# Kernel tuning notes

Hardware: AMD Instinct MI355X
Metric: run time of the kernel (lower is better)

## Reference

```python
import jax, jax.numpy as jnp
import numpy as np

B, T = 256, 2048
U = Y = 32
H = 128
Z = 64
L = 2  # GRU layers


def _mlp2(x, w1, b1, w2, b2):
    # Linear -> ReLU -> Linear (PyTorch Linear: y = x @ W.T + b)
    return jax.nn.relu(x @ w1.T + b1) @ w2.T + b2


def _gru_cell(x, h, wih, whh):
    # PyTorch GRUCell (bias=False), gate order [r, z, n]
    gi = x @ wih.T  # [B, 3H]
    gh = h @ whh.T
    i_r, i_z, i_n = jnp.split(gi, 3, axis=-1)
    h_r, h_z, h_n = jnp.split(gh, 3, axis=-1)
    r = jax.nn.sigmoid(i_r + h_r)
    z = jax.nn.sigmoid(i_z + h_z)
    n = jnp.tanh(i_n + r * h_n)
    return (1.0 - z) * n + z * h


def setup_inputs() -> dict:
    key = jax.random.key(0)
    ks = jax.random.split(key, 32)
    f32 = jnp.float32
    w = lambda k, shape: jax.random.normal(k, shape, f32) * 0.05
    inp = {
        'u': jax.random.normal(ks[0], (B, U, T), f32),
        'y': jax.random.normal(ks[1], (B, Y, T), f32),
        'h0': jax.random.uniform(ks[2], (L, B, H), f32),
        # phi_u: Linear(U,H) ReLU Linear(H,H)
        'pu_w1': w(ks[3], (H, U)), 'pu_b1': w(ks[4], (H,)),
        'pu_w2': w(ks[5], (H, H)), 'pu_b2': w(ks[6], (H,)),
        # dynn: Linear(2H,H) ReLU Linear(H,H)
        'dy_w1': w(ks[7], (H, 2 * H)), 'dy_b1': w(ks[8], (H,)),
        'dy_w2': w(ks[9], (H, H)), 'dy_b2': w(ks[10], (H,)),
        # x_mean / x_logvar heads: Linear(H,Z)
        'xm_w': w(ks[11], (Z, H)), 'xm_b': w(ks[12], (Z,)),
        'xlv_w': w(ks[13], (Z, H)), 'xlv_b': w(ks[14], (Z,)),
        # phi_x: Linear(2Z,H) ReLU Linear(H,H)
        'px_w1': w(ks[15], (H, 2 * Z)), 'px_b1': w(ks[16], (H,)),
        'px_w2': w(ks[17], (H, H)), 'px_b2': w(ks[18], (H,)),
        # menn: Linear(H,H) ReLU Linear(H,Y)
        'me_w1': w(ks[19], (H, H)), 'me_b1': w(ks[20], (H,)),
        'me_w2': w(ks[21], (Y, H)), 'me_b2': w(ks[22], (Y,)),
        # GRU (bias=False), stacked per layer: [L, 3H, H]
        'gru_wih': w(ks[23], (L, 3 * H, H)),
        'gru_whh': w(ks[24], (L, 3 * H, H)),
    }
    return inp


def reference(u, y, h0, pu_w1, pu_b1, pu_w2, pu_b2, dy_w1, dy_b1, dy_w2, dy_b2,
              xm_w, xm_b, xlv_w, xlv_b, px_w1, px_b1, px_w2, px_b2,
              me_w1, me_b1, me_w2, me_b2, gru_wih, gru_whh):
    u_seq = jnp.moveaxis(u, 2, 0)  # [T, B, U]
    y_seq = jnp.moveaxis(y, 2, 0)  # [T, B, Y]

    def step(carry, ty):
        h, loss = carry  # h: [L, B, H]
        ut, yt = ty
        phi_u = _mlp2(ut, pu_w1, pu_b1, pu_w2, pu_b2)                     # [B, H]
        dphi = _mlp2(jnp.concatenate([phi_u, h[-1]], axis=1),
                     dy_w1, dy_b1, dy_w2, dy_b2)                          # [B, H]
        x_mean = dphi @ xm_w.T + xm_b                                     # [B, Z]
        x_logvar = dphi @ xlv_w.T + xlv_b                                 # [B, Z]
        # GRU step (uses pre-update h; dynn already consumed old h[-1])
        inp = phi_u
        new_h = []
        for l in range(L):
            hl = _gru_cell(inp, h[l], gru_wih[l], gru_whh[l])
            new_h.append(hl)
            inp = hl
        h = jnp.stack(new_h)
        # mpnt_wt <= 0 branch: pure NN measurement
        phi_x = _mlp2(jnp.concatenate([x_mean, x_logvar], axis=1),
                      px_w1, px_b1, px_w2, px_b2)                         # [B, H]
        y_hat = _mlp2(phi_x, me_w1, me_b1, me_w2, me_b2)                  # [B, Y]
        loss = loss + jnp.sum((y_hat - yt) ** 2)
        return (h, loss), None

    (h, loss), _ = jax.lax.scan(step, (h0, jnp.float32(0.0)), (u_seq, y_seq))
    return loss
```

## Files before the change

kernel.cpp:

```cpp
#include <hip/hip_runtime.h>

#define DI __device__ __forceinline__

typedef unsigned short u16;
typedef unsigned int u32;
typedef unsigned long long u64;
typedef __bf16 bf16v __attribute__((ext_vector_type(8)));
typedef float f32x4 __attribute__((ext_vector_type(4)));

constexpr int B_ = 256, T_ = 2048, H_ = 128;
constexpr int BU = B_ * 32;

constexpr size_t O_PU_W1 = 0;
constexpr size_t O_PU_W2 = 4096;
constexpr size_t O_DY_W1 = 20480;
constexpr size_t O_DY_W2 = 53248;
constexpr size_t O_XM_W  = 69632;
constexpr size_t O_XLV_W = 77824;
constexpr size_t O_PX_W1 = 86016;
constexpr size_t O_PX_W2 = 102400;
constexpr size_t O_ME_W1 = 118784;
constexpr size_t O_ME_W2 = 135168;
constexpr size_t O_WIH   = 139264;
constexpr size_t O_WHH   = 237568;

constexpr size_t WS_WB   = 0;
constexpr size_t WS_HST  = 0x100000;
constexpr size_t WS_PART = 0x140000;
constexpr size_t WS_DATA = 0x180000;

DI u16 f2b(float x) {
  union { float f; unsigned u; } v; v.f = x;
  unsigned r = v.u + 0x7fffu + ((v.u >> 16) & 1u);
  return (u16)(r >> 16);
}
DI float b2f(u16 h) { union { unsigned u; float f; } v; v.u = ((unsigned)h) << 16; return v.f; }
DI float asf(u32 u) { union { unsigned u; float f; } v; v.u = u; return v.f; }
DI float sigm(float x) {
  return __builtin_amdgcn_rcpf(1.f + __builtin_amdgcn_exp2f(-1.44269504f * x));
}
DI float tanhg(float x) {
  return fmaf(2.f, __builtin_amdgcn_rcpf(1.f + __builtin_amdgcn_exp2f(-2.88539008f * x)), -1.f);
}
DI f32x4 MFMA(bf16v a, bf16v b, f32x4 c) {
  return __builtin_amdgcn_mfma_f32_16x16x32_bf16(a, b, c, 0, 0, 0);
}
DI void MFA(f32x4& c, const bf16v& a_agpr, const bf16v& b) {
  asm("v_mfma_f32_16x16x32_bf16 %0, %1, %2, %0"
      : "+v"(c) : "a"(a_agpr), "v"(b));
}
DI bf16v ldb(const u16* p) { return *reinterpret_cast<const bf16v*>(p); }
DI u32 cvtpk(float a, float b) {
  u32 d;
  asm("v_cvt_pk_bf16_f32 %0, %1, %2" : "=v"(d) : "v"(a), "v"(b));
  return d;
}
DI u64 pk4(float a, float b, float c, float d) {
  return (u64)cvtpk(a, b) | ((u64)cvtpk(c, d) << 32);
}
DI void bar_lds() {
  asm volatile("s_waitcnt lgkmcnt(0)\n\ts_barrier" ::: "memory");
}

__global__ void k_convert_weights(
    const float* pu_w1, const float* pu_w2, const float* dy_w1, const float* dy_w2,
    const float* xm_w, const float* xlv_w, const float* px_w1, const float* px_w2,
    const float* me_w1, const float* me_w2, const float* gih, const float* ghh,
    const float* h0, u16* wb, float* hst) {
  int i0 = blockIdx.x * blockDim.x + threadIdx.x;
  int st = gridDim.x * blockDim.x;
#define CVT(src, off, n) for (int i = i0; i < (n); i += st) wb[(off) + i] = f2b(src[i]);
  CVT(pu_w1, O_PU_W1, 4096)  CVT(pu_w2, O_PU_W2, 16384)
  CVT(dy_w1, O_DY_W1, 32768) CVT(dy_w2, O_DY_W2, 16384)
  CVT(xm_w,  O_XM_W,  8192)  CVT(xlv_w, O_XLV_W, 8192)
  CVT(px_w1, O_PX_W1, 16384) CVT(px_w2, O_PX_W2, 16384)
  CVT(me_w1, O_ME_W1, 16384) CVT(me_w2, O_ME_W2, 4096)
  CVT(gih,   O_WIH,   98304) CVT(ghh,   O_WHH,   98304)
#undef CVT
  for (int i = i0; i < 2 * B_ * H_; i += st) hst[i] = h0[i];
}

__global__ void k_transpose(const float* __restrict__ u, const float* __restrict__ y,
                            u16* __restrict__ uT, u16* __restrict__ yT, int t0) {
  const float* src = blockIdx.z ? y : u;
  u16* dst = blockIdx.z ? yT : uT;
  __shared__ float tile[32][33];
  const int tx = threadIdx.x, ty = threadIdx.y;
  const int c0 = blockIdx.x * 32;
  const int r0 = blockIdx.y * 32;
#pragma unroll
  for (int i = 0; i < 4; ++i)
    tile[ty + i * 8][tx] = src[(size_t)(r0 + ty + i * 8) * T_ + t0 + c0 + tx];
  __syncthreads();
#pragma unroll
  for (int i = 0; i < 4; ++i)
    dst[(size_t)(c0 + ty + i * 8) * BU + r0 + tx] = f2b(tile[tx][ty + i * 8]);
}

DI void role_gru(u16* smem, const u16* __restrict__ gi0, const u16* __restrict__ wb,
                 float* __restrict__ hst, u16* __restrict__ h1old, int TCr, int blk) {
  u16* SH0 = smem;
  u16* SH1 = smem + 4352;
  const int lane = threadIdx.x & 63, w = threadIdx.x >> 6;
  const int ln = lane & 15, lq = lane >> 4;
  const int f0 = w * 16;
  const int fme = f0 + lq * 4;
  const int b0 = blk * 16;
  const u16* wh0 = wb + O_WHH;
  const u16* wi1 = wb + O_WIH + 49152;
  const u16* wh1 = wb + O_WHH + 49152;

  bf16v wH0[3][4], wI1[3][4], wH1[3][4];
#pragma unroll
  for (int g = 0; g < 3; ++g)
#pragma unroll
    for (int kt = 0; kt < 4; ++kt) {
      size_t row = (size_t)(g * 128 + f0 + ln);
      size_t col = (size_t)kt * 32 + lq * 8;
      wH0[g][kt] = ldb(wh0 + row * H_ + col);
      wI1[g][kt] = ldb(wi1 + row * H_ + col);
      wH1[g][kt] = ldb(wh1 + row * H_ + col);
    }
#pragma unroll
  for (int g = 0; g < 3; ++g)
#pragma unroll
    for (int kt = 0; kt < 4; ++kt)
      asm volatile("" : "+a"(wH0[g][kt]), "+a"(wI1[g][kt]), "+a"(wH1[g][kt]));

  float h0s[4], h1s[4];
#pragma unroll
  for (int j = 0; j < 4; ++j) {
    h0s[j] = hst[(size_t)(0 * B_ + b0 + ln) * H_ + fme + j];
    h1s[j] = hst[(size_t)(1 * B_ + b0 + ln) * H_ + fme + j];
  }
  *reinterpret_cast<u64*>(&SH0[2176 + ln * 136 + fme]) = pk4(h0s[0], h0s[1], h0s[2], h0s[3]);
  *reinterpret_cast<u64*>(&SH1[2176 + ln * 136 + fme]) = pk4(h1s[0], h1s[1], h1s[2], h1s[3]);
  u16* hp = h1old + (size_t)(b0 + ln) * H_ + fme;
  *reinterpret_cast<u64*>(hp) = pk4(h1s[0], h1s[1], h1s[2], h1s[3]);

  const u16* gp = gi0 + (size_t)(b0 + ln) * 384 + fme;
  u64 gq0 = *reinterpret_cast<const u64*>(gp);
  u64 gq1 = *reinterpret_cast<const u64*>(gp + 128);
  u64 gq2 = *reinterpret_cast<const u64*>(gp + 256);
  gp += (size_t)B_ * 384;

  __syncthreads();

  {
    f32x4 cR = {0,0,0,0}, cZ = {0,0,0,0}, cHN = {0,0,0,0};
#pragma unroll
    for (int kt = 0; kt < 4; ++kt) {
      bf16v aH = ldb(&SH0[2176 + ln * 136 + kt * 32 + lq * 8]);
      MFA(cR,  wH0[0][kt], aH);
      MFA(cZ,  wH0[1][kt], aH);
      MFA(cHN, wH0[2][kt], aH);
    }
    u32 l0 = (u32)gq0, h0w = (u32)(gq0 >> 32);
    u32 l1 = (u32)gq1, h1w = (u32)(gq1 >> 32);
    u32 l2 = (u32)gq2, h2w = (u32)(gq2 >> 32);
    float gr[4] = {asf(l0 << 16), asf(l0 & 0xffff0000u), asf(h0w << 16), asf(h0w & 0xffff0000u)};
    float gz[4] = {asf(l1 << 16), asf(l1 & 0xffff0000u), asf(h1w << 16), asf(h1w & 0xffff0000u)};
    float gn[4] = {asf(l2 << 16), asf(l2 & 0xffff0000u), asf(h2w << 16), asf(h2w & 0xffff0000u)};
#pragma unroll
    for (int j = 0; j < 4; ++j) {
      float r = sigm(cR[j] + gr[j]);
      float z = sigm(cZ[j] + gz[j]);
      float n = tanhg(fmaf(r, cHN[j], gn[j]));
      h0s[j] = fmaf(z, h0s[j] - n, n);
    }
    *reinterpret_cast<u64*>(&SH0[0 * 2176 + ln * 136 + fme]) =
        pk4(h0s[0], h0s[1], h0s[2], h0s[3]);
    gq0 = *reinterpret_cast<const u64*>(gp);
    gq1 = *reinterpret_cast<const u64*>(gp + 128);
    gq2 = *reinterpret_cast<const u64*>(gp + 256);
    gp += (size_t)B_ * 384;
    bar_lds();
  }

#define GRU_PERIOD(H0R, H0W, DOL0, SLOT_OK, PF)                                 \
  {                                                                             \
    bf16v aH[4], aG[4];                                                         \
    _Pragma("unroll")                                                           \
    for (int kt = 0; kt < 4; ++kt) {                                            \
      aH[kt] = ldb(&SH0[(H0R) * 2176 + ln * 136 + kt * 32 + lq * 8]);           \
      aG[kt] = ldb(&SH1[(H0W) * 2176 + ln * 136 + kt * 32 + lq * 8]);           \
    }                                                                           \
    f32x4 dR = {0,0,0,0}, dZ = {0,0,0,0}, dIN = {0,0,0,0}, dHN = {0,0,0,0};     \
    _Pragma("unroll")                                                           \
    for (int kt = 0; kt < 4; ++kt) {                                            \
      MFA(dR,  wI1[0][kt], aH[kt]);  MFA(dR,  wH1[0][kt], aG[kt]);              \
      MFA(dZ,  wI1[1][kt], aH[kt]);  MFA(dZ,  wH1[1][kt], aG[kt]);              \
      MFA(dIN, wI1[2][kt], aH[kt]);  MFA(dHN, wH1[2][kt], aG[kt]);              \
    }                                                                           \
    if (DOL0) {                                                                 \
      f32x4 cR = {0,0,0,0}, cZ = {0,0,0,0}, cHN = {0,0,0,0};                    \
      _Pragma("unroll")                                                         \
      for (int kt = 0; kt < 4; ++kt) {                                          \
        MFA(cR,  wH0[0][kt], aH[kt]);                                           \
        MFA(cZ,  wH0[1][kt], aH[kt]);                                           \
        MFA(cHN, wH0[2][kt], aH[kt]);                                           \
      }                                                                         \
      u32 l0 = (u32)gq0, h0w = (u32)(gq0 >> 32);                                \
      u32 l1 = (u32)gq1, h1w = (u32)(gq1 >> 32);                                \
      u32 l2 = (u32)gq2, h2w = (u32)(gq2 >> 32);                                \
      float gr[4] = {asf(l0 << 16), asf(l0 & 0xffff0000u),                      \
                     asf(h0w << 16), asf(h0w & 0xffff0000u)};                   \
      float gz[4] = {asf(l1 << 16), asf(l1 & 0xffff0000u),                      \
                     asf(h1w << 16), asf(h1w & 0xffff0000u)};                   \
      float gn[4] = {asf(l2 << 16), asf(l2 & 0xffff0000u),                      \
                     asf(h2w << 16), asf(h2w & 0xffff0000u)};                   \
      _Pragma("unroll")                                                         \
      for (int j = 0; j < 4; ++j) {                                             \
        float r = sigm(cR[j] + gr[j]);                                          \
        float z = sigm(cZ[j] + gz[j]);                                          \
        float n = tanhg(fmaf(r, cHN[j], gn[j]));                                \
        h0s[j] = fmaf(z, h0s[j] - n, n);                                        \
      }                                                                         \
      *reinterpret_cast<u64*>(&SH0[(H0W) * 2176 + ln * 136 + fme]) =            \
          pk4(h0s[0], h0s[1], h0s[2], h0s[3]);                                  \
    }                                                                           \
    {                                                                           \
      _Pragma("unroll")                                                         \
      for (int j = 0; j < 4; ++j) {                                             \
        float r = sigm(dR[j]);                                                  \
        float z = sigm(dZ[j]);                                                  \
        float n = tanhg(fmaf(r, dHN[j], dIN[j]));                               \
        h1s[j] = fmaf(z, h1s[j] - n, n);                                        \
      }                                                                         \
      u64 q = pk4(h1s[0], h1s[1], h1s[2], h1s[3]);                              \
      *reinterpret_cast<u64*>(&SH1[(H0R) * 2176 + ln * 136 + fme]) = q;         \
      if (SLOT_OK) {                                                            \
        hp += (size_t)B_ * H_;                                                  \
        *reinterpret_cast<u64*>(hp) = q;                                        \
      }                                                                         \
    }                                                                           \
    if (PF) {                                                                   \
      gq0 = *reinterpret_cast<const u64*>(gp);                                  \
      gq1 = *reinterpret_cast<const u64*>(gp + 128);                            \
      gq2 = *reinterpret_cast<const u64*>(gp + 256);                            \
      gp += (size_t)B_ * 384;                                                   \
    }                                                                           \
    bar_lds();                                                                  \
  }

  for (int s = 1; s <= TCr; s += 2) {
    GRU_PERIOD(0, 1, true, true, (s + 1 < TCr))
    GRU_PERIOD(1, 0, (s + 1 < TCr), (s + 1 < TCr), (s + 2 < TCr))
  }
#undef GRU_PERIOD

#pragma unroll
  for (int j = 0; j < 4; ++j) {
    hst[(size_t)(0 * B_ + b0 + ln) * H_ + fme + j] = h0s[j];
    hst[(size_t)(1 * B_ + b0 + ln) * H_ + fme + j] = h1s[j];
  }
}

DI void layer128(const u16* __restrict__ W, const float* __restrict__ bias,
                 const u16* A, u16* Dst, int dstOff, int nTiles, bool relu,
                 int ln, int lq) {
  bf16v a[2][4];
#pragma unroll
  for (int mt = 0; mt < 2; ++mt)
#pragma unroll
    for (int kt = 0; kt < 4; ++kt)
      a[mt][kt] = ldb(A + (mt * 16 + ln) * 136 + kt * 32 + lq * 8);
  for (int nt = 0; nt < nTiles; ++nt) {
    f32x4 c0 = {0,0,0,0}, c1 = {0,0,0,0};
#pragma unroll
    for (int kt = 0; kt < 4; ++kt) {
      bf16v b = ldb(W + (nt * 16 + ln) * 128 + kt * 32 + lq * 8);
      c0 = MFMA(a[0][kt], b, c0); c1 = MFMA(a[1][kt], b, c1);
    }
    float bv = bias[nt * 16 + ln];
#pragma unroll
    for (int mt = 0; mt < 2; ++mt)
#pragma unroll
      for (int j = 0; j < 4; ++j) {
        float v = (mt ? c1[j] : c0[j]) + bv;
        if (relu) v = fmaxf(v, 0.f);
        Dst[(mt * 16 + lq * 4 + j) * 136 + dstOff + nt * 16 + ln] = f2b(v);
      }
  }
}

DI void role_post(u16* smem, const u16* __restrict__ phiu, const u16* __restrict__ h1old,
                  const u16* __restrict__ yT, const u16* __restrict__ wb,
                  const float* dy_b1, const float* dy_b2, const float* xm_b,
                  const float* xlv_b, const float* px_b1, const float* px_b2,
                  const float* me_b1, const float* me_b2,
                  float* __restrict__ partials, int first, int blk) {
  const int lane = threadIdx.x & 63, w = threadIdx.x >> 6;
  const int ln = lane & 15, lq = lane >> 4;
  const int r0 = (blk * 8 + w) * 32;
  u16* X = smem + w * 8704;
  u16* Yb = X + 4352;
  float* wsum = (float*)(smem + 69632);

  {
    bf16v a[2][8];
#pragma unroll
    for (int mt = 0; mt < 2; ++mt)
#pragma unroll
      for (int kt = 0; kt < 8; ++kt) {
        size_t row = (size_t)(r0 + mt * 16 + ln);
        a[mt][kt] = (kt < 4) ? ldb(phiu + row * H_ + kt * 32 + lq * 8)
                             : ldb(h1old + row * H_ + (kt - 4) * 32 + lq * 8);
      }
    const u16* W = wb + O_DY_W1;
    for (int nt = 0; nt < 8; ++nt) {
      f32x4 c0 = {0,0,0,0}, c1 = {0,0,0,0};
#pragma unroll
      for (int kt = 0; kt < 8; ++kt) {
        bf16v b = ldb(W + (nt * 16 + ln) * 256 + kt * 32 + lq * 8);
        c0 = MFMA(a[0][kt], b, c0); c1 = MFMA(a[1][kt], b, c1);
      }
      float bv = dy_b1[nt * 16 + ln];
#pragma unroll
      for (int mt = 0; mt < 2; ++mt)
#pragma unroll
        for (int j = 0; j < 4; ++j) {
          float v = (mt ? c1[j] : c0[j]) + bv;
          X[(mt * 16 + lq * 4 + j) * 136 + nt * 16 + ln] = f2b(fmaxf(v, 0.f));
        }
    }
  }
  layer128(wb + O_DY_W2, dy_b2, X, Yb, 0, 8, false, ln, lq);
  layer128(wb + O_XM_W,  xm_b,  Yb, X, 0, 4, false, ln, lq);
  layer128(wb + O_XLV_W, xlv_b, Yb, X, 64, 4, false, ln, lq);
  layer128(wb + O_PX_W1, px_b1, X, Yb, 0, 8, true,  ln, lq);
  layer128(wb + O_PX_W2, px_b2, Yb, X, 0, 8, false, ln, lq);
  layer128(wb + O_ME_W1, me_b1, X, Yb, 0, 8, true,  ln, lq);

  float lsum = 0.f;
  {
    bf16v a[2][4];
#pragma unroll
    for (int mt = 0; mt < 2; ++mt)
#pragma unroll
      for (int kt = 0; kt < 4; ++kt)
        a[mt][kt] = ldb(Yb + (mt * 16 + ln) * 136 + kt * 32 + lq * 8);
    const u16* W = wb + O_ME_W2;
#pragma unroll
    for (int nt = 0; nt < 2; ++nt) {
      f32x4 c0 = {0,0,0,0}, c1 = {0,0,0,0};
#pragma unroll
      for (int kt = 0; kt < 4; ++kt) {
        bf16v b = ldb(W + (nt * 16 + ln) * 128 + kt * 32 + lq * 8);
        c0 = MFMA(a[0][kt], b, c0); c1 = MFMA(a[1][kt], b, c1);
      }
      float bv = me_b2[nt * 16 + ln];
#pragma unroll
      for (int mt = 0; mt < 2; ++mt)
#pragma unroll
        for (int j = 0; j < 4; ++j) {
          int m = mt * 16 + lq * 4 + j;
          float v = (mt ? c1[j] : c0[j]) + bv;
          float yv = b2f(yT[(size_t)(r0 + m) * 32 + nt * 16 + ln]);
          float d = v - yv;
          lsum += d * d;
        }
    }
  }
#pragma unroll
  for (int o = 32; o; o >>= 1) lsum += __shfl_down(lsum, o);
  if (lane == 0) wsum[w] = lsum;
  __syncthreads();
  if (threadIdx.x == 0) {
    float v = 0.f;
#pragma unroll
    for (int i = 0; i < 8; ++i) v += wsum[i];
    if (first) partials[blk] = v;
    else       partials[blk] += v;
  }
}

DI void role_phiu(u16* smem, const u16* __restrict__ uT, const u16* __restrict__ wb,
                  const float* __restrict__ pu_b1, const float* __restrict__ pu_b2,
                  u16* __restrict__ phiu, u16* __restrict__ gi0, int blk) {
  const int lane = threadIdx.x & 63, w = threadIdx.x >> 6;
  const int ln = lane & 15, lq = lane >> 4;
  const int r0 = (blk * 8 + w) * 32;
  u16* hb  = smem + w * 4352;
  u16* hb2 = smem + 34816 + w * 4352;

  bf16v a0 = ldb(uT + (size_t)(r0 + ln) * 32 + lq * 8);
  bf16v a1 = ldb(uT + (size_t)(r0 + 16 + ln) * 32 + lq * 8);
  const u16* w1 = wb + O_PU_W1;
#pragma unroll
  for (int nt = 0; nt < 8; ++nt) {
    f32x4 c0 = {0.f, 0.f, 0.f, 0.f}, c1 = {0.f, 0.f, 0.f, 0.f};
    bf16v b = ldb(w1 + (nt * 16 + ln) * 32 + lq * 8);
    c0 = MFMA(a0, b, c0); c1 = MFMA(a1, b, c1);
    float bv = pu_b1[nt * 16 + ln];
#pragma unroll
    for (int j = 0; j < 4; ++j) {
      hb[(lq * 4 + j) * 136 + nt * 16 + ln]      = f2b(fmaxf(c0[j] + bv, 0.f));
      hb[(16 + lq * 4 + j) * 136 + nt * 16 + ln] = f2b(fmaxf(c1[j] + bv, 0.f));
    }
  }
  bf16v a[2][4];
#pragma unroll
  for (int mt = 0; mt < 2; ++mt)
#pragma unroll
    for (int kt = 0; kt < 4; ++kt)
      a[mt][kt] = ldb(hb + (mt * 16 + ln) * 136 + kt * 32 + lq * 8);
  const u16* w2 = wb + O_PU_W2;
#pragma unroll
  for (int nt = 0; nt < 8; ++nt) {
    f32x4 c0 = {0.f, 0.f, 0.f, 0.f}, c1 = {0.f, 0.f, 0.f, 0.f};
#pragma unroll
    for (int kt = 0; kt < 4; ++kt) {
      bf16v b = ldb(w2 + (nt * 16 + ln) * 128 + kt * 32 + lq * 8);
      c0 = MFMA(a[0][kt], b, c0); c1 = MFMA(a[1][kt], b, c1);
    }
    float bv = pu_b2[nt * 16 + ln];
#pragma unroll
    for (int mt = 0; mt < 2; ++mt)
#pragma unroll
      for (int j = 0; j < 4; ++j) {
        float v = (mt ? c1[j] : c0[j]) + bv;
        hb2[(mt * 16 + lq * 4 + j) * 136 + nt * 16 + ln] = f2b(v);
      }
  }
  __syncthreads();

#pragma unroll
  for (int i = 0; i < 16; ++i) {
    int idx = lane + 64 * i;
    int row = idx >> 5, c4 = idx & 31;
    u64 v = *reinterpret_cast<const u64*>(&hb2[row * 136 + c4 * 4]);
    *reinterpret_cast<u64*>(&phiu[(size_t)(r0 + row) * 128 + c4 * 4]) = v;
  }

  bf16v bP[2][4];
#pragma unroll
  for (int bh = 0; bh < 2; ++bh)
#pragma unroll
    for (int kt = 0; kt < 4; ++kt)
      bP[bh][kt] = ldb(&hb2[(bh * 16 + ln) * 136 + kt * 32 + lq * 8]);
  const u16* wih0 = wb + O_WIH;
  for (int nt = 0; nt < 24; ++nt) {
    bf16v aW[4];
#pragma unroll
    for (int kt = 0; kt < 4; ++kt)
      aW[kt] = ldb(wih0 + (size_t)(nt * 16 + ln) * 128 + kt * 32 + lq * 8);
#pragma unroll
    for (int bh = 0; bh < 2; ++bh) {
      f32x4 c = {0.f, 0.f, 0.f, 0.f};
#pragma unroll
      for (int kt = 0; kt < 4; ++kt) c = MFMA(aW[kt], bP[bh][kt], c);
      u64 q = pk4(c[0], c[1], c[2], c[3]);
      *reinterpret_cast<u64*>(
          &gi0[(size_t)(r0 + bh * 16 + ln) * 384 + nt * 16 + lq * 4]) = q;
    }
  }
}

DI void role_transpose(u16* smem, const float* __restrict__ u, const float* __restrict__ y,
                       u16* __restrict__ uT, u16* __restrict__ yT, int t0, int blk, int TCr) {
  float* tile = (float*)smem;
  const int worker = threadIdx.x >> 8;
  const int tid = threadIdx.x & 255;
  const int tx = tid & 31, ty = tid >> 5;
  float* tl = tile + worker * (32 * 33);
  const int ntt = TCr / 32;
  for (int i = 0; i < 4; ++i) {
    int gtile = blk * 8 + worker * 4 + i;
    int tt = gtile % ntt;
    int rest = gtile / ntt;
    int rr = rest & 255, uy = rest >> 8;
    const float* src = uy ? y : u;
    u16* dst = uy ? yT : uT;
    int c0 = tt * 32, r0 = rr * 32;
#pragma unroll
    for (int k = 0; k < 4; ++k)
      tl[(ty + k * 8) * 33 + tx] = src[(size_t)(r0 + ty + k * 8) * T_ + t0 + c0 + tx];
    __syncthreads();
#pragma unroll
    for (int k = 0; k < 4; ++k)
      dst[(size_t)(c0 + ty + k * 8) * BU + r0 + tx] = f2b(tl[tx * 33 + ty + k * 8]);
    __syncthreads();
  }
}

__global__ __launch_bounds__(512, 2) void k_mega(
    const float* u, const float* yy,
    const u16* uT_r, u16* uT_w, u16* yT_w, const u16* yT_r,
    const u16* phiu_r, u16* phiu_w,
    const u16* gi0_r, u16* gi0_w,
    const u16* h1_r, u16* h1_w,
    const u16* wb, float* hst,
    const float* pu_b1, const float* pu_b2,
    const float* dy_b1, const float* dy_b2, const float* xm_b, const float* xlv_b,
    const float* px_b1, const float* px_b2, const float* me_b1, const float* me_b2,
    float* partials, int first,
    int TCr, int nG, int nP, int nU, int t0T) {
  __shared__ __align__(16) u16 smem[69664];
  int b = blockIdx.x;
  if (b < nG) { role_gru(smem, gi0_r, wb, hst, h1_w, TCr, b); return; }
  b -= nG;
  if (b < nP) {
    role_post(smem, phiu_r, h1_r, yT_r, wb, dy_b1, dy_b2, xm_b, xlv_b,
              px_b1, px_b2, me_b1, me_b2, partials, first, b);
    return;
  }
  b -= nP;
  if (b < nU) { role_phiu(smem, uT_r, wb, pu_b1, pu_b2, phiu_w, gi0_w, b); return; }
  b -= nU;
  role_transpose(smem, u, yy, uT_w, yT_w, t0T, b, TCr);
}

__global__ void k_finalize(const float* __restrict__ partials, float* __restrict__ out,
                           int nPart) {
  __shared__ double s[256];
  double acc = 0.0;
  for (int i = threadIdx.x; i < nPart; i += 256) acc += (double)partials[i];
  s[threadIdx.x] = acc;
  __syncthreads();
  for (int o = 128; o; o >>= 1) {
    if (threadIdx.x < o) s[threadIdx.x] += s[threadIdx.x + o];
    __syncthreads();
  }
  if (threadIdx.x == 0) out[0] = (float)s[0];
}

extern "C" void kernel_launch(void* const* d_in, const int* in_sizes, int n_in,
                              void* d_out, int out_size, void* d_ws, size_t ws_size,
                              hipStream_t stream) {
  const float* u     = (const float*)d_in[0];
  const float* y     = (const float*)d_in[1];
  const float* h0    = (const float*)d_in[2];
  const float* pu_w1 = (const float*)d_in[3];
  const float* pu_b1 = (const float*)d_in[4];
  const float* pu_w2 = (const float*)d_in[5];
  const float* pu_b2 = (const float*)d_in[6];
  const float* dy_w1 = (const float*)d_in[7];
  const float* dy_b1 = (const float*)d_in[8];
  const float* dy_w2 = (const float*)d_in[9];
  const float* dy_b2 = (const float*)d_in[10];
  const float* xm_w  = (const float*)d_in[11];
  const float* xm_b  = (const float*)d_in[12];
  const float* xlv_w = (const float*)d_in[13];
  const float* xlv_b = (const float*)d_in[14];
  const float* px_w1 = (const float*)d_in[15];
  const float* px_b1 = (const float*)d_in[16];
  const float* px_w2 = (const float*)d_in[17];
  const float* px_b2 = (const float*)d_in[18];
  const float* me_w1 = (const float*)d_in[19];
  const float* me_b1 = (const float*)d_in[20];
  const float* me_w2 = (const float*)d_in[21];
  const float* me_b2 = (const float*)d_in[22];
  const float* gih   = (const float*)d_in[23];
  const float* ghh   = (const float*)d_in[24];

  int TC = 64;
  for (int cand : {256, 128}) {
    size_t ut = (size_t)cand * B_ * 32 * 2;
    size_t ph = (size_t)cand * B_ * 128 * 2;
    size_t gi = (size_t)cand * B_ * 384 * 2;
    if (WS_DATA + 6 * ut + 5 * ph + 2 * gi <= ws_size) { TC = cand; break; }
  }
  const int NCH = T_ / TC;
  const int RC = TC * B_;
  size_t ut_b = (size_t)RC * 32 * 2, ph_b = (size_t)RC * 128 * 2, gi_b = (size_t)RC * 384 * 2;

  char* ws = (char*)d_ws;
  u16* wb    = (u16*)(ws + WS_WB);
  float* hst = (float*)(ws + WS_HST);
  float* prt = (float*)(ws + WS_PART);
  char* p = ws + WS_DATA;
  u16* uTb[2]; u16* yTb[4]; u16* phb[3]; u16* h1b[2]; u16* gib[2];
  for (int i = 0; i < 2; ++i) { uTb[i] = (u16*)p; p += ut_b; }
  for (int i = 0; i < 4; ++i) { yTb[i] = (u16*)p; p += ut_b; }
  for (int i = 0; i < 3; ++i) { phb[i] = (u16*)p; p += ph_b; }
  for (int i = 0; i < 2; ++i) { h1b[i] = (u16*)p; p += ph_b; }
  for (int i = 0; i < 2; ++i) { gib[i] = (u16*)p; p += gi_b; }
  float* out = (float*)d_out;

  const int nPostB = RC / 256;
  const int nPhiB  = RC / 256;
  const int nTrB   = (TC / 32) * 64;

  k_convert_weights<<<256, 256, 0, stream>>>(pu_w1, pu_w2, dy_w1, dy_w2, xm_w, xlv_w,
                                             px_w1, px_w2, me_w1, me_w2, gih, ghh,
                                             h0, wb, hst);
  k_transpose<<<dim3(TC / 32, 256, 2), dim3(32, 8), 0, stream>>>(u, y, uTb[0], yTb[0], 0);
  if (NCH > 1)
    k_transpose<<<dim3(TC / 32, 256, 2), dim3(32, 8), 0, stream>>>(u, y, uTb[1], yTb[1], TC);
  k_mega<<<nPhiB, 512, 0, stream>>>(u, y, uTb[0], uTb[0], yTb[0], yTb[0],
                                    phb[0], phb[0], gib[0], gib[0], h1b[0], h1b[0],
                                    wb, hst, pu_b1, pu_b2, dy_b1, dy_b2, xm_b, xlv_b,
                                    px_b1, px_b2, me_b1, me_b2, prt, 0,
                                    TC, 0, 0, nPhiB, 0);
  for (int c = 0; c <= NCH; ++c) {
    int nG = (c < NCH) ? 16 : 0;
    int nP = (c >= 1) ? nPostB : 0;
    int nU = (c + 1 < NCH) ? nPhiB : 0;
    int nT = (c + 2 < NCH) ? nTrB : 0;
    int grid = nG + nP + nU + nT;
    if (!grid) continue;
    k_mega<<<grid, 512, 0, stream>>>(
        u, y,
        uTb[(c + 1) & 1], uTb[(c + 2) & 1], yTb[(c + 2) & 3],
        yTb[c >= 1 ? (c - 1) & 3 : 0],
        phb[c >= 1 ? (c - 1) % 3 : 0], phb[(c + 1) % 3],
        gib[c & 1], gib[(c + 1) & 1],
        h1b[c >= 1 ? (c - 1) & 1 : 0], h1b[c & 1],
        wb, hst, pu_b1, pu_b2, dy_b1, dy_b2, xm_b, xlv_b,
        px_b1, px_b2, me_b1, me_b2,
        prt, (c == 1) ? 1 : 0,
        TC, nG, nP, nU, (c + 2) * TC);
  }
  k_finalize<<<1, 256, 0, stream>>>(prt, out, nPostB);
}
```

Before: 2.752 ms.

## Split GRU layers into separate producer/consumer blocks synchronized via global flags

The two GRU layers, previously computed together in each recurrence block, now run in separate workgroups. Sixteen layer-0 blocks compute h0 and publish it to a global buffer with a release flag per step. Sixteen layer-1 blocks spin on that flag and consume h0 from global memory. This shortens the serial per-step critical path and spreads register and MFMA load across twice as many CUs. In exchange it adds global-memory round trips and spin-wait latency per step, plus a deadlock risk if the producer blocks are not co-resident with the consumers.

```diff
diff --git a/kernel.cpp b/kernel.cpp
--- a/kernel.cpp
+++ b/kernel.cpp
@@ -27,6 +27,7 @@
 constexpr size_t WS_WB   = 0;
 constexpr size_t WS_HST  = 0x100000;
 constexpr size_t WS_PART = 0x140000;
+constexpr size_t WS_FLAG = 0x150000;
 constexpr size_t WS_DATA = 0x180000;
 
 DI u16 f2b(float x) {
@@ -66,7 +67,7 @@
     const float* pu_w1, const float* pu_w2, const float* dy_w1, const float* dy_w2,
     const float* xm_w, const float* xlv_w, const float* px_w1, const float* px_w2,
     const float* me_w1, const float* me_w2, const float* gih, const float* ghh,
-    const float* h0, u16* wb, float* hst) {
+    const float* h0, u16* wb, float* hst, u32* flags) {
   int i0 = blockIdx.x * blockDim.x + threadIdx.x;
   int st = gridDim.x * blockDim.x;
 #define CVT(src, off, n) for (int i = i0; i < (n); i += st) wb[(off) + i] = f2b(src[i]);
@@ -78,6 +79,7 @@
   CVT(gih,   O_WIH,   98304) CVT(ghh,   O_WHH,   98304)
 #undef CVT
   for (int i = i0; i < 2 * B_ * H_; i += st) hst[i] = h0[i];
+  for (int i = i0; i < 16; i += st) flags[i] = 0;
 }
 
 __global__ void k_transpose(const float* __restrict__ u, const float* __restrict__ y,
@@ -97,46 +99,34 @@
     dst[(size_t)(c0 + ty + i * 8) * BU + r0 + tx] = f2b(tile[tx][ty + i * 8]);
 }
 
-DI void role_gru(u16* smem, const u16* __restrict__ gi0, const u16* __restrict__ wb,
-                 float* __restrict__ hst, u16* __restrict__ h1old, int TCr, int blk) {
+DI void role_gru0(u16* smem, const u16* __restrict__ gi0, const u16* __restrict__ wb,
+                  float* __restrict__ hst, u16* __restrict__ h0x, u32* flags,
+                  int pbase, int TCr, int blk) {
   u16* SH0 = smem;
-  u16* SH1 = smem + 4352;
   const int lane = threadIdx.x & 63, w = threadIdx.x >> 6;
   const int ln = lane & 15, lq = lane >> 4;
   const int f0 = w * 16;
   const int fme = f0 + lq * 4;
   const int b0 = blk * 16;
   const u16* wh0 = wb + O_WHH;
-  const u16* wi1 = wb + O_WIH + 49152;
-  const u16* wh1 = wb + O_WHH + 49152;
-
-  bf16v wH0[3][4], wI1[3][4], wH1[3][4];
+
+  bf16v wH0[3][4];
 #pragma unroll
   for (int g = 0; g < 3; ++g)
 #pragma unroll
-    for (int kt = 0; kt < 4; ++kt) {
-      size_t row = (size_t)(g * 128 + f0 + ln);
-      size_t col = (size_t)kt * 32 + lq * 8;
-      wH0[g][kt] = ldb(wh0 + row * H_ + col);
-      wI1[g][kt] = ldb(wi1 + row * H_ + col);
-      wH1[g][kt] = ldb(wh1 + row * H_ + col);
-    }
+    for (int kt = 0; kt < 4; ++kt)
+      wH0[g][kt] = ldb(wh0 + (size_t)(g * 128 + f0 + ln) * H_ + kt * 32 + lq * 8);
 #pragma unroll
   for (int g = 0; g < 3; ++g)
 #pragma unroll
     for (int kt = 0; kt < 4; ++kt)
-      asm volatile("" : "+a"(wH0[g][kt]), "+a"(wI1[g][kt]), "+a"(wH1[g][kt]));
-
-  float h0s[4], h1s[4];
-#pragma unroll
-  for (int j = 0; j < 4; ++j) {
+      asm volatile("" : "+a"(wH0[g][kt]));
+
+  float h0s[4];
+#pragma unroll
+  for (int j = 0; j < 4; ++j)
     h0s[j] = hst[(size_t)(0 * B_ + b0 + ln) * H_ + fme + j];
-    h1s[j] = hst[(size_t)(1 * B_ + b0 + ln) * H_ + fme + j];
-  }
   *reinterpret_cast<u64*>(&SH0[2176 + ln * 136 + fme]) = pk4(h0s[0], h0s[1], h0s[2], h0s[3]);
-  *reinterpret_cast<u64*>(&SH1[2176 + ln * 136 + fme]) = pk4(h1s[0], h1s[1], h1s[2], h1s[3]);
-  u16* hp = h1old + (size_t)(b0 + ln) * H_ + fme;
-  *reinterpret_cast<u64*>(hp) = pk4(h1s[0], h1s[1], h1s[2], h1s[3]);
 
   const u16* gp = gi0 + (size_t)(b0 + ln) * 384 + fme;
   u64 gq0 = *reinterpret_cast<const u64*>(gp);
@@ -146,14 +136,19 @@
 
   __syncthreads();
 
-  {
+  u16* rd = SH0 + 2176;
+  u16* wr = SH0;
+  for (int s = 0; s < TCr; ++s) {
+    bf16v aH[4];
+#pragma unroll
+    for (int kt = 0; kt < 4; ++kt)
+      aH[kt] = ldb(&rd[ln * 136 + kt * 32 + lq * 8]);
     f32x4 cR = {0,0,0,0}, cZ = {0,0,0,0}, cHN = {0,0,0,0};
 #pragma unroll
     for (int kt = 0; kt < 4; ++kt) {
-      bf16v aH = ldb(&SH0[2176 + ln * 136 + kt * 32 + lq * 8]);
-      MFA(cR,  wH0[0][kt], aH);
-      MFA(cZ,  wH0[1][kt], aH);
-      MFA(cHN, wH0[2][kt], aH);
+      MFA(cR,  wH0[0][kt], aH[kt]);
+      MFA(cZ,  wH0[1][kt], aH[kt]);
+      MFA(cHN, wH0[2][kt], aH[kt]);
     }
     u32 l0 = (u32)gq0, h0w = (u32)(gq0 >> 32);
     u32 l1 = (u32)gq1, h1w = (u32)(gq1 >> 32);
@@ -168,92 +163,127 @@
       float n = tanhg(fmaf(r, cHN[j], gn[j]));
       h0s[j] = fmaf(z, h0s[j] - n, n);
     }
-    *reinterpret_cast<u64*>(&SH0[0 * 2176 + ln * 136 + fme]) =
-        pk4(h0s[0], h0s[1], h0s[2], h0s[3]);
-    gq0 = *reinterpret_cast<const u64*>(gp);
-    gq1 = *reinterpret_cast<const u64*>(gp + 128);
-    gq2 = *reinterpret_cast<const u64*>(gp + 256);
-    gp += (size_t)B_ * 384;
+    u64 q = pk4(h0s[0], h0s[1], h0s[2], h0s[3]);
+    __hip_atomic_store(
+        (unsigned long long*)(h0x + (size_t)s * B_ * H_ + (size_t)(b0 + ln) * H_ + fme),
+        q, __ATOMIC_RELAXED, __HIP_MEMORY_SCOPE_AGENT);
+    *reinterpret_cast<u64*>(&wr[ln * 136 + fme]) = q;
+    __syncthreads();
+    if (threadIdx.x == 0)
+      __hip_atomic_store(&flags[blk], (u32)(pbase + s + 1),
+                         __ATOMIC_RELEASE, __HIP_MEMORY_SCOPE_AGENT);
+    if (s + 1 < TCr) {
+      gq0 = *reinterpret_cast<const u64*>(gp);
+      gq1 = *reinterpret_cast<const u64*>(gp + 128);
+      gq2 = *reinterpret_cast<const u64*>(gp + 256);
+      gp += (size_t)B_ * 384;
+    }
+    u16* tmp = rd; rd = wr; wr = tmp;
+  }
+#pragma unroll
+  for (int j = 0; j < 4; ++j)
+    hst[(size_t)(0 * B_ + b0 + ln) * H_ + fme + j] = h0s[j];
+}
+
+DI void role_gru1(u16* smem, const u16* __restrict__ wb,
+                  float* __restrict__ hst, u16* __restrict__ h1old,
+                  const u16* __restrict__ h0x, u32* flags,
+                  int pbase, int TCr, int blk) {
+  u16* SH1 = smem;
+  const int lane = threadIdx.x & 63, w = threadIdx.x >> 6;
+  const int ln = lane & 15, lq = lane >> 4;
+  const int f0 = w * 16;
+  const int fme = f0 + lq * 4;
+  const int b0 = blk * 16;
+  const u16* wi1 = wb + O_WIH + 49152;
+  const u16* wh1 = wb + O_WHH + 49152;
+
+  bf16v wI1[3][4], wH1[3][4];
+#pragma unroll
+  for (int g = 0; g < 3; ++g)
+#pragma unroll
+    for (int kt = 0; kt < 4; ++kt) {
+      size_t row = (size_t)(g * 128 + f0 + ln);
+      size_t col = (size_t)kt * 32 + lq * 8;
+      wI1[g][kt] = ldb(wi1 + row * H_ + col);
+      wH1[g][kt] = ldb(wh1 + row * H_ + col);
+    }
+#pragma unroll
+  for (int g = 0; g < 3; ++g)
+#pragma unroll
+    for (int kt = 0; kt < 4; ++kt)
+      asm volatile("" : "+a"(wI1[g][kt]), "+a"(wH1[g][kt]));
+
+  float h1s[4];
+#pragma unroll
+  for (int j = 0; j < 4; ++j)
+    h1s[j] = hst[(size_t)(1 * B_ + b0 + ln) * H_ + fme + j];
+  u64 qi = pk4(h1s[0], h1s[1], h1s[2], h1s[3]);
+  *reinterpret_cast<u64*>(&SH1[2176 + ln * 136 + fme]) = qi;
+  u16* hp = h1old + (size_t)(b0 + ln) * H_ + fme;
+  *reinterpret_cast<u64*>(hp) = qi;
+
+  __syncthreads();
+
+  u16* rd = SH1 + 2176;
+  u16* wr = SH1;
+  u32 seen = 0;
+  for (int s = 1; s <= TCr; ++s) {
+    u32 want = (u32)(pbase + s);
+    if (seen < want) {
+      do {
+        seen = __hip_atomic_load(&flags[blk], __ATOMIC_RELAXED, __HIP_MEMORY_SCOPE_AGENT);
+      } while (seen < want);
+      __builtin_amdgcn_fence(__ATOMIC_ACQUIRE, "agent");
+    }
+    const unsigned long long* hsrc = (const unsigned long long*)
+        (h0x + (size_t)(s - 1) * B_ * H_ + (size_t)(b0 + ln) * H_);
+    bf16v aH[4];
+#pragma unroll
+    for (int kt = 0; kt < 4; ++kt) {
+      union { u64 q[2]; bf16v v; } t;
+      t.q[0] = __hip_atomic_load((unsigned long long*)(hsrc + kt * 8 + lq * 2),
+                                 __ATOMIC_RELAXED, __HIP_MEMORY_SCOPE_AGENT);
+      t.q[1] = __hip_atomic_load((unsigned long long*)(hsrc + kt * 8 + lq * 2 + 1),
+                                 __ATOMIC_RELAXED, __HIP_MEMORY_SCOPE_AGENT);
+      aH[kt] = t.v;
+    }
+    bf16v aG[4];
+#pragma unroll
+    for (int kt = 0; kt < 4; ++kt)
+      aG[kt] = ldb(&rd[ln * 136 + kt * 32 + lq * 8]);
+    f32x4 dR = {0,0,0,0}, dZ = {0,0,0,0}, dIN = {0,0,0,0}, dHN = {0,0,0,0};
+#pragma unroll
+    for (int kt = 0; kt < 4; ++kt) {
+      MFA(dR,  wH1[0][kt], aG[kt]);
+      MFA(dZ,  wH1[1][kt], aG[kt]);
+      MFA(dHN, wH1[2][kt], aG[kt]);
+    }
+#pragma unroll
+    for (int kt = 0; kt < 4; ++kt) {
+      MFA(dR,  wI1[0][kt], aH[kt]);
+      MFA(dZ,  wI1[1][kt], aH[kt]);
+      MFA(dIN, wI1[2][kt], aH[kt]);
+    }
+#pragma unroll
+    for (int j = 0; j < 4; ++j) {
+      float r = sigm(dR[j]);
+      float z = sigm(dZ[j]);
+      float n = tanhg(fmaf(r, dHN[j], dIN[j]));
+      h1s[j] = fmaf(z, h1s[j] - n, n);
+    }
+    u64 q = pk4(h1s[0], h1s[1], h1s[2], h1s[3]);
+    *reinterpret_cast<u64*>(&wr[ln * 136 + fme]) = q;
+    if (s < TCr) {
+      hp += (size_t)B_ * H_;
+      *reinterpret_cast<u64*>(hp) = q;
+    }
     bar_lds();
-  }
-
-#define GRU_PERIOD(H0R, H0W, DOL0, SLOT_OK, PF)                                 \
-  {                                                                             \
-    bf16v aH[4], aG[4];                                                         \
-    _Pragma("unroll")                                                           \
-    for (int kt = 0; kt < 4; ++kt) {                                            \
-      aH[kt] = ldb(&SH0[(H0R) * 2176 + ln * 136 + kt * 32 + lq * 8]);           \
-      aG[kt] = ldb(&SH1[(H0W) * 2176 + ln * 136 + kt * 32 + lq * 8]);           \
-    }                                                                           \
-    f32x4 dR = {0,0,0,0}, dZ = {0,0,0,0}, dIN = {0,0,0,0}, dHN = {0,0,0,0};     \
-    _Pragma("unroll")                                                           \
-    for (int kt = 0; kt < 4; ++kt) {                                            \
-      MFA(dR,  wI1[0][kt], aH[kt]);  MFA(dR,  wH1[0][kt], aG[kt]);              \
-      MFA(dZ,  wI1[1][kt], aH[kt]);  MFA(dZ,  wH1[1][kt], aG[kt]);              \
-      MFA(dIN, wI1[2][kt], aH[kt]);  MFA(dHN, wH1[2][kt], aG[kt]);              \
-    }                                                                           \
-    if (DOL0) {                                                                 \
-      f32x4 cR = {0,0,0,0}, cZ = {0,0,0,0}, cHN = {0,0,0,0};                    \
-      _Pragma("unroll")                                                         \
-      for (int kt = 0; kt < 4; ++kt) {                                          \
-        MFA(cR,  wH0[0][kt], aH[kt]);                                           \
-        MFA(cZ,  wH0[1][kt], aH[kt]);                                           \
-        MFA(cHN, wH0[2][kt], aH[kt]);                                           \
-      }                                                                         \
-      u32 l0 = (u32)gq0, h0w = (u32)(gq0 >> 32);                                \
-      u32 l1 = (u32)gq1, h1w = (u32)(gq1 >> 32);                                \
-      u32 l2 = (u32)gq2, h2w = (u32)(gq2 >> 32);                                \
-      float gr[4] = {asf(l0 << 16), asf(l0 & 0xffff0000u),                      \
-                     asf(h0w << 16), asf(h0w & 0xffff0000u)};                   \
-      float gz[4] = {asf(l1 << 16), asf(l1 & 0xffff0000u),                      \
-                     asf(h1w << 16), asf(h1w & 0xffff0000u)};                   \
-      float gn[4] = {asf(l2 << 16), asf(l2 & 0xffff0000u),                      \
-                     asf(h2w << 16), asf(h2w & 0xffff0000u)};                   \
-      _Pragma("unroll")                                                         \
-      for (int j = 0; j < 4; ++j) {                                             \
-        float r = sigm(cR[j] + gr[j]);                                          \
-        float z = sigm(cZ[j] + gz[j]);                                          \
-        float n = tanhg(fmaf(r, cHN[j], gn[j]));                                \
-        h0s[j] = fmaf(z, h0s[j] - n, n);                                        \
-      }                                                                         \
-      *reinterpret_cast<u64*>(&SH0[(H0W) * 2176 + ln * 136 + fme]) =            \
-          pk4(h0s[0], h0s[1], h0s[2], h0s[3]);                                  \
-    }                                                                           \
-    {                                                                           \
-      _Pragma("unroll")                                                         \
-      for (int j = 0; j < 4; ++j) {                                             \
-        float r = sigm(dR[j]);                                                  \
-        float z = sigm(dZ[j]);                                                  \
-        float n = tanhg(fmaf(r, dHN[j], dIN[j]));                               \
-        h1s[j] = fmaf(z, h1s[j] - n, n);                                        \
-      }                                                                         \
-      u64 q = pk4(h1s[0], h1s[1], h1s[2], h1s[3]);                              \
-      *reinterpret_cast<u64*>(&SH1[(H0R) * 2176 + ln * 136 + fme]) = q;         \
-      if (SLOT_OK) {                                                            \
-        hp += (size_t)B_ * H_;                                                  \
-        *reinterpret_cast<u64*>(hp) = q;                                        \
-      }                                                                         \
-    }                                                                           \
-    if (PF) {                                                                   \
-      gq0 = *reinterpret_cast<const u64*>(gp);                                  \
-      gq1 = *reinterpret_cast<const u64*>(gp + 128);                            \
-      gq2 = *reinterpret_cast<const u64*>(gp + 256);                            \
-      gp += (size_t)B_ * 384;                                                   \
-    }                                                                           \
-    bar_lds();                                                                  \
-  }
-
-  for (int s = 1; s <= TCr; s += 2) {
-    GRU_PERIOD(0, 1, true, true, (s + 1 < TCr))
-    GRU_PERIOD(1, 0, (s + 1 < TCr), (s + 1 < TCr), (s + 2 < TCr))
-  }
-#undef GRU_PERIOD
-
-#pragma unroll
-  for (int j = 0; j < 4; ++j) {
-    hst[(size_t)(0 * B_ + b0 + ln) * H_ + fme + j] = h0s[j];
+    u16* tmp = rd; rd = wr; wr = tmp;
+  }
+#pragma unroll
+  for (int j = 0; j < 4; ++j)
     hst[(size_t)(1 * B_ + b0 + ln) * H_ + fme + j] = h1s[j];
-  }
 }
 
 DI void layer128(const u16* __restrict__ W, const float* __restrict__ bias,
@@ -490,6 +520,7 @@
     const u16* phiu_r, u16* phiu_w,
     const u16* gi0_r, u16* gi0_w,
     const u16* h1_r, u16* h1_w,
+    u16* h0x, u32* flags, int pbase,
     const u16* wb, float* hst,
     const float* pu_b1, const float* pu_b2,
     const float* dy_b1, const float* dy_b2, const float* xm_b, const float* xlv_b,
@@ -498,7 +529,11 @@
     int TCr, int nG, int nP, int nU, int t0T) {
   __shared__ __align__(16) u16 smem[69664];
   int b = blockIdx.x;
-  if (b < nG) { role_gru(smem, gi0_r, wb, hst, h1_w, TCr, b); return; }
+  if (b < nG) {
+    if (b < 16) role_gru0(smem, gi0_r, wb, hst, h0x, flags, pbase, TCr, b);
+    else        role_gru1(smem, wb, hst, h1_w, h0x, flags, pbase, TCr, b - 16);
+    return;
+  }
   b -= nG;
   if (b < nP) {
     role_post(smem, phiu_r, h1_r, yT_r, wb, dy_b1, dy_b2, xm_b, xlv_b,
@@ -559,7 +594,7 @@
     size_t ut = (size_t)cand * B_ * 32 * 2;
     size_t ph = (size_t)cand * B_ * 128 * 2;
     size_t gi = (size_t)cand * B_ * 384 * 2;
-    if (WS_DATA + 6 * ut + 5 * ph + 2 * gi <= ws_size) { TC = cand; break; }
+    if (WS_DATA + 6 * ut + 6 * ph + 2 * gi <= ws_size) { TC = cand; break; }
   }
   const int NCH = T_ / TC;
   const int RC = TC * B_;
@@ -569,13 +604,15 @@
   u16* wb    = (u16*)(ws + WS_WB);
   float* hst = (float*)(ws + WS_HST);
   float* prt = (float*)(ws + WS_PART);
+  u32* flg   = (u32*)(ws + WS_FLAG);
   char* p = ws + WS_DATA;
-  u16* uTb[2]; u16* yTb[4]; u16* phb[3]; u16* h1b[2]; u16* gib[2];
+  u16* uTb[2]; u16* yTb[4]; u16* phb[3]; u16* h1b[2]; u16* gib[2]; u16* h0x;
   for (int i = 0; i < 2; ++i) { uTb[i] = (u16*)p; p += ut_b; }
   for (int i = 0; i < 4; ++i) { yTb[i] = (u16*)p; p += ut_b; }
   for (int i = 0; i < 3; ++i) { phb[i] = (u16*)p; p += ph_b; }
   for (int i = 0; i < 2; ++i) { h1b[i] = (u16*)p; p += ph_b; }
   for (int i = 0; i < 2; ++i) { gib[i] = (u16*)p; p += gi_b; }
+  h0x = (u16*)p; p += ph_b;
   float* out = (float*)d_out;
 
   const int nPostB = RC / 256;
@@ -584,17 +621,18 @@
 
   k_convert_weights<<<256, 256, 0, stream>>>(pu_w1, pu_w2, dy_w1, dy_w2, xm_w, xlv_w,
                                              px_w1, px_w2, me_w1, me_w2, gih, ghh,
-                                             h0, wb, hst);
+                                             h0, wb, hst, flg);
   k_transpose<<<dim3(TC / 32, 256, 2), dim3(32, 8), 0, stream>>>(u, y, uTb[0], yTb[0], 0);
   if (NCH > 1)
     k_transpose<<<dim3(TC / 32, 256, 2), dim3(32, 8), 0, stream>>>(u, y, uTb[1], yTb[1], TC);
   k_mega<<<nPhiB, 512, 0, stream>>>(u, y, uTb[0], uTb[0], yTb[0], yTb[0],
                                     phb[0], phb[0], gib[0], gib[0], h1b[0], h1b[0],
+                                    h0x, flg, 0,
                                     wb, hst, pu_b1, pu_b2, dy_b1, dy_b2, xm_b, xlv_b,
                                     px_b1, px_b2, me_b1, me_b2, prt, 0,
                                     TC, 0, 0, nPhiB, 0);
   for (int c = 0; c <= NCH; ++c) {
-    int nG = (c < NCH) ? 16 : 0;
+    int nG = (c < NCH) ? 32 : 0;
     int nP = (c >= 1) ? nPostB : 0;
     int nU = (c + 1 < NCH) ? nPhiB : 0;
     int nT = (c + 2 < NCH) ? nTrB : 0;
@@ -607,6 +645,7 @@
         phb[c >= 1 ? (c - 1) % 3 : 0], phb[(c + 1) % 3],
         gib[c & 1], gib[(c + 1) & 1],
         h1b[c >= 1 ? (c - 1) & 1 : 0], h1b[c & 1],
+        h0x, flg, c * TC,
         wb, hst, pu_b1, pu_b2, dy_b1, dy_b2, xm_b, xlv_b,
         px_b1, px_b2, me_b1, me_b2,
         prt, (c == 1) ? 1 : 0,
```

New measurement: 5.113 ms. 1.86x slower.
